# Kernel tuning notes

Hardware: AMD Instinct MI355X
Metric: run time of the kernel (lower is better)

The kernel has to match this reference:

```python
import jax, jax.numpy as jnp
import numpy as np
from jax import lax

PAD = 1  # 3x3 conv, stride 1, padding 1


def conv2d(x, w, b=None):
    # x: [B,C,H,W], w: [O,I,3,3]
    y = lax.conv_general_dilated(x, w, window_strides=(1, 1),
                                 padding=((PAD, PAD), (PAD, PAD)),
                                 dimension_numbers=("NCHW", "OIHW", "NCHW"))
    if b is not None:
        y = y + b[None, :, None, None]
    return y


def _bilinear(img, py, px):
    # img: [C,H,W]; py,px: [K,H,W] sampling coords (float). Zero padding outside.
    H, W = img.shape[1], img.shape[2]
    y0 = jnp.floor(py)
    x0 = jnp.floor(px)
    wy = py - y0  # [K,H,W]
    wx = px - x0
    y0i = y0.astype(jnp.int32)
    x0i = x0.astype(jnp.int32)

    def gather(yi, xi):
        valid = ((yi >= 0) & (yi < H) & (xi >= 0) & (xi < W)).astype(img.dtype)
        yc = jnp.clip(yi, 0, H - 1)
        xc = jnp.clip(xi, 0, W - 1)
        return img[:, yc, xc] * valid[None]  # [C,K,H,W]

    v00 = gather(y0i, x0i)
    v01 = gather(y0i, x0i + 1)
    v10 = gather(y0i + 1, x0i)
    v11 = gather(y0i + 1, x0i + 1)
    return (v00 * (1 - wy) * (1 - wx) + v01 * (1 - wy) * wx
            + v10 * wy * (1 - wx) + v11 * wy * wx)  # [C,K,H,W]


def reference(x, w_offset, b_offset, w_mask, b_mask, w_conv):
    B, C, H, W = x.shape
    K = 9  # 3x3 kernel taps
    offset = conv2d(x, w_offset, b_offset)              # [B,2K,H,W]
    mask = jax.nn.sigmoid(conv2d(x, w_mask, b_mask))    # [B,K,H,W]

    off = offset.reshape(B, K, 2, H, W)
    dy = off[:, :, 0]  # [B,K,H,W] (torchvision layout: y first)
    dx = off[:, :, 1]

    k = jnp.arange(K)
    ky = (k // 3).astype(x.dtype) - PAD  # tap row offset in {-1,0,1}
    kx = (k % 3).astype(x.dtype) - PAD
    ii = jnp.arange(H, dtype=x.dtype)
    jj = jnp.arange(W, dtype=x.dtype)

    py = ii[None, None, :, None] + ky[None, :, None, None] + dy  # [B,K,H,W]
    px = jj[None, None, None, :] + kx[None, :, None, None] + dx

    sampled = jax.vmap(_bilinear)(x, py, px)  # [B,C,K,H,W]
    sampled = sampled * mask[:, None]          # modulated deform-conv v2

    # weight [64,3,3,3] -> [O,C,K]; contract over C and kernel taps
    out = jnp.einsum('bckhw,ock->bohw', sampled, w_conv.reshape(w_conv.shape[0], C, K))
    return out


def setup_inputs() -> dict:
    key = jax.random.key(0)
    k = jax.random.split(key, 6)
    B, C, H, W = 16, 3, 256, 256
    return {
        'x': jax.random.normal(k[0], (B, C, H, W), jnp.float32),
        'w_offset': jax.random.normal(k[1], (18, 3, 3, 3), jnp.float32) * 0.1,
        'b_offset': jax.random.normal(k[2], (18,), jnp.float32) * 0.1,
        'w_mask': jax.random.normal(k[3], (9, 3, 3, 3), jnp.float32) * 0.1,
        'b_mask': jax.random.normal(k[4], (9,), jnp.float32) * 0.1,
        'w_conv': jax.random.normal(k[5], (64, 3, 3, 3), jnp.float32) * 0.1,
    }
```

## Files before the change

### kernel.cpp

```cpp
#include <hip/hip_runtime.h>
#include <hip/hip_bf16.h>

#define HH 256
#define WW 256
#define CC 3
#define KK 9
#define OC 64
#define KD 27
#define PSTS 40
#define WRB 5120
#define XST (4 * WRB)
#define XSLOT 1024
#define ROWS 2
#define SLOTS 8

typedef __attribute__((ext_vector_type(8))) short bf16x8;
typedef __attribute__((ext_vector_type(4))) short s16x4;
typedef __attribute__((ext_vector_type(4))) float f32x4;
typedef __attribute__((ext_vector_type(2))) float f32x2;
typedef __attribute__((ext_vector_type(2))) unsigned int u32x2;
typedef __attribute__((ext_vector_type(4))) unsigned int u32x4;

static __device__ __forceinline__ short f2bf(float f) {
    __hip_bfloat16 h = __float2bfloat16(f);
    return __builtin_bit_cast(short, h);
}
static __device__ __forceinline__ unsigned pack2(short a, short b) {
    return (unsigned)(unsigned short)a | ((unsigned)(unsigned short)b << 16);
}
static __device__ __forceinline__ float bf2f(unsigned w) {
    return __uint_as_float(w << 16);
}
static __device__ __forceinline__ float bfup(unsigned w) {
    return __uint_as_float(w & 0xffff0000u);
}
static __device__ __forceinline__ unsigned q8(float z) {
    float s = 1.0f / (1.0f + __expf(-z));
    return (unsigned)__builtin_rintf(s * 255.0f);
}

__global__ __launch_bounds__(256) void dcn_prep(
    const float* __restrict__ x,
    const float* __restrict__ w_offset, const float* __restrict__ b_offset,
    const float* __restrict__ w_mask,   const float* __restrict__ b_mask,
    const float* __restrict__ w_conv,
    short* __restrict__ xbf, short* __restrict__ wcf, char* __restrict__ wof,
    int npix)
{
    const int tid = threadIdx.x;
    if (blockIdx.x == gridDim.x - 1) {
        if (tid < 64) {
            const int fm = tid & 15, kc = tid >> 4;
#pragma unroll
            for (int t = 0; t < 4; ++t) {
                bf16x8 v;
#pragma unroll
                for (int e = 0; e < 8; ++e) {
                    int kd = kc * 8 + e;
                    v[e] = (kd < KD) ? f2bf(w_conv[(t * 16 + fm) * KD + kd]) : (short)0;
                }
                *(bf16x8*)(wcf + tid * 32 + t * 8) = v;
            }
#pragma unroll
            for (int t = 0; t < 2; ++t) {
                int ch = t * 16 + fm;
                bf16x8 vh, vl;
#pragma unroll
                for (int e = 0; e < 8; ++e) {
                    int kd = kc * 8 + e;
                    float val = 0.0f;
                    if (kd < KD) {
                        if (ch < 18) val = w_offset[ch * KD + kd];
                        else if (ch < KD) val = w_mask[(ch - 18) * KD + kd];
                    }
                    unsigned u = __float_as_uint(val);
                    vh[e] = (short)(u >> 16);
                    float d = val - __uint_as_float(u & 0xffff0000u);
                    vl[e] = (short)(__float_as_uint(d) >> 16);
                }
                *(bf16x8*)(wof + tid * 96 + t * 16) = vh;
                *(bf16x8*)(wof + tid * 96 + 32 + t * 16) = vl;
            }
#pragma unroll
            for (int t = 0; t < 2; ++t) {
                f32x4 cb;
#pragma unroll
                for (int r = 0; r < 4; ++r) {
                    int ch = t * 16 + kc * 4 + r;
                    float v = 0.0f;
                    if (ch < 18) v = b_offset[ch];
                    else if (ch < KD) v = b_mask[ch - 18];
                    cb[r] = v;
                }
                *(f32x4*)(wof + tid * 96 + 64 + t * 16) = cb;
            }
        }
        return;
    }

    const int p0 = (blockIdx.x * 256 + tid) * 4;
    if (p0 >= npix) return;
    const int bb = p0 >> 16;
    const int q  = p0 & 0xffff;
    const float* xb = x + (size_t)bb * (3 * 65536) + q;
    f32x4 r0 = *(const f32x4*)(xb);
    f32x4 r1 = *(const f32x4*)(xb + 65536);
    f32x4 r2 = *(const f32x4*)(xb + 131072);

    bf16x8 v0 = {f2bf(r0[0]), f2bf(r1[0]), f2bf(r2[0]), 0,
                 f2bf(r0[1]), f2bf(r1[1]), f2bf(r2[1]), 0};
    bf16x8 v1 = {f2bf(r0[2]), f2bf(r1[2]), f2bf(r2[2]), 0,
                 f2bf(r0[3]), f2bf(r1[3]), f2bf(r2[3]), 0};
    short* A = xbf + (size_t)p0 * 4;
    *(bf16x8*)A       = v0;
    *(bf16x8*)(A + 8) = v1;
}

__global__ __launch_bounds__(256, 4) void dcn_main(
    const float* __restrict__ x,
    const short* __restrict__ xbf,
    const short* __restrict__ wcf,
    const char*  __restrict__ wof,
    float* __restrict__ out)
{
    __shared__ __align__(16) char LDSBUF[XST + SLOTS * XSLOT * 2];

    const int tid = threadIdx.x;
    const int j = tid;
    const int r0 = (blockIdx.x & 127) * ROWS;
    const int b = blockIdx.x >> 7;
    const int lane = tid & 63;
    const int wv = tid >> 6;
    const int fm = lane & 15;
    const int kc = lane >> 4;

    char* wbase = LDSBUF + wv * WRB;
    short* patchS = (short*)wbase;
    short* xs = (short*)(LDSBUF + XST);

    const float* xb = x + (size_t)b * (CC * HH * WW);
    const short* xrow = xbf + (size_t)b * (HH * WW * 4);

    {
        u32x2 st[SLOTS];
#pragma unroll
        for (int s = 0; s < SLOTS; ++s) {
            int gr = min(max(r0 - 3 + s, 0), HH - 1);
            st[s] = *(const u32x2*)(xrow + ((size_t)gr * WW + tid) * 4);
        }
#pragma unroll
        for (int s = 0; s < SLOTS; ++s) {
            *(u32x2*)(xs + s * XSLOT + tid * 4) = st[s];
        }
    }
    __syncthreads();

    const char* wl = wof + lane * 96;
    bf16x8 whi0 = *(const bf16x8*)(wl);
    bf16x8 whi1 = *(const bf16x8*)(wl + 16);
    bf16x8 wlo0 = *(const bf16x8*)(wl + 32);
    bf16x8 wlo1 = *(const bf16x8*)(wl + 48);
    f32x4 cb0 = *(const f32x4*)(wl + 64);
    f32x4 cb1 = *(const f32x4*)(wl + 80);
    bf16x8 afrag[4];
#pragma unroll
    for (int t2 = 0; t2 < 4; ++t2) afrag[t2] = *(const bf16x8*)(wcf + lane * 32 + t2 * 8);

    const float* x0p = xb;
    const float* x1p = xb + (size_t)HH * WW;
    const float* x2p = xb + (size_t)2 * HH * WW;

#pragma unroll 1
    for (int d = 0; d < ROWS; ++d) {
        const int ri = r0 + d;

        const bool yok0 = (ri - 1) >= 0, yok2 = (ri + 1) < HH;
        const bool xok0 = (j - 1) >= 0, xok2 = (j + 1) < WW;
        s16x4 pr[3][3];
#pragma unroll
        for (int p = 0; p < 3; ++p) {
#pragma unroll
            for (int q = 0; q < 3; ++q) {
                int xx = min(max(j + q - 1, 0), WW - 1);
                pr[p][q] = *(const s16x4*)(xs + (d + p + 2) * XSLOT + xx * 4);
            }
        }
        {
            short* rp = patchS + lane * PSTS;
#pragma unroll
            for (int o = 0; o < 4; ++o) {
                bf16x8 vh;
#pragma unroll
                for (int e = 0; e < 8; ++e) {
                    int kd = o * 8 + e;
                    if (kd < KD) {
                        int c = kd / 9, rem = kd - c * 9, p = rem / 3, q = rem - p * 3;
                        bool ok = (p == 0 ? yok0 : (p == 2 ? yok2 : true)) &&
                                  (q == 0 ? xok0 : (q == 2 ? xok2 : true));
                        vh[e] = ok ? pr[p][q][c] : (short)0;
                    } else {
                        vh[e] = (short)0;
                    }
                }
                *(bf16x8*)(rp + o * 8) = vh;
            }
        }

        f32x4 dacc[4][2];
#pragma unroll
        for (int g = 0; g < 4; ++g) {
            bf16x8 phi = *(const bf16x8*)(patchS + (g * 16 + fm) * PSTS + kc * 8);
            f32x4 a0 = __builtin_amdgcn_mfma_f32_16x16x32_bf16(whi0, phi, cb0, 0, 0, 0);
            a0 = __builtin_amdgcn_mfma_f32_16x16x32_bf16(wlo0, phi, a0, 0, 0, 0);
            f32x4 a1 = __builtin_amdgcn_mfma_f32_16x16x32_bf16(whi1, phi, cb1, 0, 0, 0);
            a1 = __builtin_amdgcn_mfma_f32_16x16x32_bf16(wlo1, phi, a1, 0, 0, 0);
            dacc[g][0] = a0;
            dacc[g][1] = a1;
        }
#pragma unroll
        for (int g = 0; g < 4; ++g) {
            int r = g * 16 + fm;
            char* dr = wbase + r * 80;
            *(f32x4*)(dr + kc * 16) = dacc[g][0];
            f32x4 a1 = dacc[g][1];
            if (kc == 0) {
                *(unsigned*)(dr + 64) = pack2(f2bf(a1[0]), f2bf(a1[1]));
                *(unsigned short*)(dr + 68) = (unsigned short)(q8(a1[2]) | (q8(a1[3]) << 8));
            } else if (kc == 1) {
                *(unsigned short*)(dr + 70) = (unsigned short)(q8(a1[0]) | (q8(a1[1]) << 8));
                *(unsigned short*)(dr + 72) = (unsigned short)(q8(a1[2]) | (q8(a1[3]) << 8));
            } else if (kc == 2) {
                *(unsigned short*)(dr + 74) = (unsigned short)(q8(a1[0]) | (q8(a1[1]) << 8));
                *(unsigned short*)(dr + 76) = (unsigned short)q8(a1[2]);
            }
        }

        const char* myD = wbase + lane * 80;
        f32x4 d03 = *(const f32x4*)(myD);
        f32x4 d47 = *(const f32x4*)(myD + 16);
        f32x4 d8b = *(const f32x4*)(myD + 32);
        f32x4 dcf = *(const f32x4*)(myD + 48);
        u32x4 tail = *(const u32x4*)(myD + 64);

        const float dyv[9] = {d03[0], d03[2], d47[0], d47[2], d8b[0], d8b[2], dcf[0], dcf[2],
                              bf2f(tail.x)};
        const float dxv[9] = {d03[1], d03[3], d47[1], d47[3], d8b[1], d8b[3], dcf[1], dcf[3],
                              bfup(tail.x)};
        const unsigned mqv[9] = {tail.y & 255u, (tail.y >> 8) & 255u, (tail.y >> 16) & 255u,
                                 tail.y >> 24, tail.z & 255u, (tail.z >> 8) & 255u,
                                 (tail.z >> 16) & 255u, tail.z >> 24, tail.w & 255u};

        float s27[KD];
#pragma unroll
        for (int k = 0; k < KK; ++k) {
            float dy = dyv[k], dx = dxv[k];
            float msk = (float)mqv[k] * (1.0f / 255.0f);

            float py = (float)(ri + (k / 3) - 1) + dy;
            float px = (float)(j + (k % 3) - 1) + dx;
            float y0f = floorf(py), x0f = floorf(px);
            float wy = py - y0f, wx = px - x0f;
            int y0 = (int)y0f, x0 = (int)x0f;
            int y1 = y0 + 1, x1 = x0 + 1;

            float w00 = (1.0f - wy) * (1.0f - wx);
            float w01 = (1.0f - wy) * wx;
            float w10 = wy * (1.0f - wx);
            float w11 = wy * wx;

            bool v0y = (unsigned)y0 < HH, v1y = (unsigned)y1 < HH;
            bool v0x = (unsigned)x0 < WW, v1x = (unsigned)x1 < WW;
            float f00 = (v0y && v0x) ? w00 : 0.0f;
            float f01 = (v0y && v1x) ? w01 : 0.0f;
            float f10 = (v1y && v0x) ? w10 : 0.0f;
            float f11 = (v1y && v1x) ? w11 : 0.0f;

            int y0c = min(max(y0, 0), HH - 1), y1c = min(max(y1, 0), HH - 1);
            int s0 = y0c - r0 + 3;
            int s1 = y1c - r0 + 3;
            float r0v_, r1v_, r2v_;
            if (__builtin_expect(__any(((unsigned)s0 > (SLOTS - 1)) ||
                                       ((unsigned)s1 > (SLOTS - 1))), 0)) {
                int x0c = min(max(x0, 0), WW - 1), x1c = min(max(x1, 0), WW - 1);
                int o00 = y0c * WW + x0c, o01 = y0c * WW + x1c;
                int o10 = y1c * WW + x0c, o11 = y1c * WW + x1c;
                r0v_ = x0p[o00] * f00 + x0p[o01] * f01 + x0p[o10] * f10 + x0p[o11] * f11;
                r1v_ = x1p[o00] * f00 + x1p[o01] * f01 + x1p[o10] * f10 + x1p[o11] * f11;
                r2v_ = x2p[o00] * f00 + x2p[o01] * f01 + x2p[o10] * f10 + x2p[o11] * f11;
            } else {
                int xl = min(max(x0, 0), WW - 2);
                bool sw = (x0 != xl);
                const short* p0 = xs + s0 * XSLOT + xl * 4;
                const short* p1 = xs + s1 * XSLOT + xl * 4;
                u32x2 lo0 = *(const u32x2*)p0;
                u32x2 hi0 = *(const u32x2*)(p0 + 4);
                u32x2 lo1 = *(const u32x2*)p1;
                u32x2 hi1 = *(const u32x2*)(p1 + 4);

                float a0 = sw ? f01 : f00, b0 = sw ? f00 : f01;
                float a1w = sw ? f11 : f10, b1w = sw ? f10 : f11;

                r0v_ = fmaf(bf2f(lo0.x), a0, fmaf(bf2f(hi0.x), b0,
                       fmaf(bf2f(lo1.x), a1w, bf2f(hi1.x) * b1w)));
                r1v_ = fmaf(bfup(lo0.x), a0, fmaf(bfup(hi0.x), b0,
                       fmaf(bfup(lo1.x), a1w, bfup(hi1.x) * b1w)));
                r2v_ = fmaf(bf2f(lo0.y), a0, fmaf(bf2f(hi0.y), b0,
                       fmaf(bf2f(lo1.y), a1w, bf2f(hi1.y) * b1w)));
            }
            s27[k]      = r0v_ * msk;
            s27[9 + k]  = r1v_ * msk;
            s27[18 + k] = r2v_ * msk;
        }

        {
            short* srow = patchS + lane * PSTS;
#pragma unroll
            for (int o = 0; o < 4; ++o) {
                bf16x8 v;
#pragma unroll
                for (int e = 0; e < 8; ++e) {
                    int kd = o * 8 + e;
                    v[e] = (kd < KD) ? f2bf(s27[kd]) : (short)0;
                }
                *(bf16x8*)(srow + o * 8) = v;
            }
        }

        float* obase = out + ((size_t)b * OC * HH + ri) * WW;
#pragma unroll
        for (int g = 0; g < 4; ++g) {
            bf16x8 sfrag = *(const bf16x8*)(patchS + (g * 16 + fm) * PSTS + kc * 8);
#pragma unroll
            for (int t2 = 0; t2 < 4; ++t2) {
                f32x4 acc = (f32x4){0.f, 0.f, 0.f, 0.f};
                acc = __builtin_amdgcn_mfma_f32_16x16x32_bf16(sfrag, afrag[t2], acc, 0, 0, 0);
                float* op = obase + (size_t)(t2 * 16 + fm) * (HH * WW) + (wv * 64 + g * 16 + kc * 4);
                *(f32x4*)op = acc;
            }
        }
    }
}

extern "C" void kernel_launch(void* const* d_in, const int* in_sizes, int n_in,
                              void* d_out, int out_size, void* d_ws, size_t ws_size,
                              hipStream_t stream) {
    const float* x        = (const float*)d_in[0];
    const float* w_offset = (const float*)d_in[1];
    const float* b_offset = (const float*)d_in[2];
    const float* w_mask   = (const float*)d_in[3];
    const float* b_mask   = (const float*)d_in[4];
    const float* w_conv   = (const float*)d_in[5];
    float* out = (float*)d_out;

    int B = in_sizes[0] / (CC * HH * WW);
    int npix = B * HH * WW;

    short* xbf = (short*)d_ws;
    short* wcf = (short*)((char*)d_ws + (size_t)npix * 8);
    char*  wof = (char*)d_ws + (size_t)npix * 8 + 4096;

    int nb = (npix + 1023) / 1024;
    hipLaunchKernelGGL(dcn_prep, dim3(nb + 1), dim3(256), 0, stream,
                       x, w_offset, b_offset, w_mask, b_mask, w_conv,
                       xbf, wcf, wof, npix);
    hipLaunchKernelGGL(dcn_main, dim3(B * (HH / ROWS)), dim3(256), 0, stream,
                       x, xbf, wcf, wof, out);
}
```

Before: 72.37 us.

## Process both rows concurrently with 512-thread blocks instead of a serial row loop

Before, each 256-thread block handled two output rows in a serial loop. Now blocks have 512 threads and each half of the block handles one row, so the row loop is gone. The halo load is split so each half stages four of the eight LDS slots. Per-wave scratch in LDS doubles to cover eight waves, which raises shared memory per block. Larger blocks with more LDS may reduce how many blocks fit on a CU, trading serial latency inside a block for more parallelism within it.

```diff
diff --git a/kernel.cpp b/kernel.cpp
--- a/kernel.cpp
+++ b/kernel.cpp
@@ -9,9 +9,9 @@
 #define KD 27
 #define PSTS 40
 #define WRB 5120
-#define XST (4 * WRB)
+#define NWAVES 8
+#define XST (NWAVES * WRB)
 #define XSLOT 1024
-#define ROWS 2
 #define SLOTS 8
 
 typedef __attribute__((ext_vector_type(8))) short bf16x8;
@@ -75,8 +75,8 @@
                     }
                     unsigned u = __float_as_uint(val);
                     vh[e] = (short)(u >> 16);
-                    float d = val - __uint_as_float(u & 0xffff0000u);
-                    vl[e] = (short)(__float_as_uint(d) >> 16);
+                    float dd = val - __uint_as_float(u & 0xffff0000u);
+                    vl[e] = (short)(__float_as_uint(dd) >> 16);
                 }
                 *(bf16x8*)(wof + tid * 96 + t * 16) = vh;
                 *(bf16x8*)(wof + tid * 96 + 32 + t * 16) = vl;
@@ -116,7 +116,7 @@
     *(bf16x8*)(A + 8) = v1;
 }
 
-__global__ __launch_bounds__(256, 4) void dcn_main(
+__global__ __launch_bounds__(512, 4) void dcn_main(
     const float* __restrict__ x,
     const short* __restrict__ xbf,
     const short* __restrict__ wcf,
@@ -126,9 +126,11 @@
     __shared__ __align__(16) char LDSBUF[XST + SLOTS * XSLOT * 2];
 
     const int tid = threadIdx.x;
-    const int j = tid;
-    const int r0 = (blockIdx.x & 127) * ROWS;
+    const int d = tid >> 8;
+    const int j = tid & 255;
+    const int r0 = (blockIdx.x & 127) * 2;
     const int b = blockIdx.x >> 7;
+    const int ri = r0 + d;
     const int lane = tid & 63;
     const int wv = tid >> 6;
     const int fm = lane & 15;
@@ -142,15 +144,16 @@
     const short* xrow = xbf + (size_t)b * (HH * WW * 4);
 
     {
-        u32x2 st[SLOTS];
-#pragma unroll
-        for (int s = 0; s < SLOTS; ++s) {
-            int gr = min(max(r0 - 3 + s, 0), HH - 1);
-            st[s] = *(const u32x2*)(xrow + ((size_t)gr * WW + tid) * 4);
-        }
-#pragma unroll
-        for (int s = 0; s < SLOTS; ++s) {
-            *(u32x2*)(xs + s * XSLOT + tid * 4) = st[s];
+        u32x2 st[4];
+#pragma unroll
+        for (int s = 0; s < 4; ++s) {
+            int slot = d * 4 + s;
+            int gr = min(max(r0 - 3 + slot, 0), HH - 1);
+            st[s] = *(const u32x2*)(xrow + ((size_t)gr * WW + j) * 4);
+        }
+#pragma unroll
+        for (int s = 0; s < 4; ++s) {
+            *(u32x2*)(xs + (d * 4 + s) * XSLOT + j * 4) = st[s];
         }
     }
     __syncthreads();
@@ -170,10 +173,7 @@
     const float* x1p = xb + (size_t)HH * WW;
     const float* x2p = xb + (size_t)2 * HH * WW;
 
-#pragma unroll 1
-    for (int d = 0; d < ROWS; ++d) {
-        const int ri = r0 + d;
-
+    {
         const bool yok0 = (ri - 1) >= 0, yok2 = (ri + 1) < HH;
         const bool xok0 = (j - 1) >= 0, xok2 = (j + 1) < WW;
         s16x4 pr[3][3];
@@ -185,158 +185,156 @@
                 pr[p][q] = *(const s16x4*)(xs + (d + p + 2) * XSLOT + xx * 4);
             }
         }
-        {
-            short* rp = patchS + lane * PSTS;
-#pragma unroll
-            for (int o = 0; o < 4; ++o) {
-                bf16x8 vh;
-#pragma unroll
-                for (int e = 0; e < 8; ++e) {
-                    int kd = o * 8 + e;
-                    if (kd < KD) {
-                        int c = kd / 9, rem = kd - c * 9, p = rem / 3, q = rem - p * 3;
-                        bool ok = (p == 0 ? yok0 : (p == 2 ? yok2 : true)) &&
-                                  (q == 0 ? xok0 : (q == 2 ? xok2 : true));
-                        vh[e] = ok ? pr[p][q][c] : (short)0;
-                    } else {
-                        vh[e] = (short)0;
-                    }
+        short* rp = patchS + lane * PSTS;
+#pragma unroll
+        for (int o = 0; o < 4; ++o) {
+            bf16x8 vh;
+#pragma unroll
+            for (int e = 0; e < 8; ++e) {
+                int kd = o * 8 + e;
+                if (kd < KD) {
+                    int c = kd / 9, rem = kd - c * 9, p = rem / 3, q = rem - p * 3;
+                    bool ok = (p == 0 ? yok0 : (p == 2 ? yok2 : true)) &&
+                              (q == 0 ? xok0 : (q == 2 ? xok2 : true));
+                    vh[e] = ok ? pr[p][q][c] : (short)0;
+                } else {
+                    vh[e] = (short)0;
                 }
-                *(bf16x8*)(rp + o * 8) = vh;
-            }
-        }
-
-        f32x4 dacc[4][2];
-#pragma unroll
-        for (int g = 0; g < 4; ++g) {
-            bf16x8 phi = *(const bf16x8*)(patchS + (g * 16 + fm) * PSTS + kc * 8);
-            f32x4 a0 = __builtin_amdgcn_mfma_f32_16x16x32_bf16(whi0, phi, cb0, 0, 0, 0);
-            a0 = __builtin_amdgcn_mfma_f32_16x16x32_bf16(wlo0, phi, a0, 0, 0, 0);
-            f32x4 a1 = __builtin_amdgcn_mfma_f32_16x16x32_bf16(whi1, phi, cb1, 0, 0, 0);
-            a1 = __builtin_amdgcn_mfma_f32_16x16x32_bf16(wlo1, phi, a1, 0, 0, 0);
-            dacc[g][0] = a0;
-            dacc[g][1] = a1;
-        }
-#pragma unroll
-        for (int g = 0; g < 4; ++g) {
-            int r = g * 16 + fm;
-            char* dr = wbase + r * 80;
-            *(f32x4*)(dr + kc * 16) = dacc[g][0];
-            f32x4 a1 = dacc[g][1];
-            if (kc == 0) {
-                *(unsigned*)(dr + 64) = pack2(f2bf(a1[0]), f2bf(a1[1]));
-                *(unsigned short*)(dr + 68) = (unsigned short)(q8(a1[2]) | (q8(a1[3]) << 8));
-            } else if (kc == 1) {
-                *(unsigned short*)(dr + 70) = (unsigned short)(q8(a1[0]) | (q8(a1[1]) << 8));
-                *(unsigned short*)(dr + 72) = (unsigned short)(q8(a1[2]) | (q8(a1[3]) << 8));
-            } else if (kc == 2) {
-                *(unsigned short*)(dr + 74) = (unsigned short)(q8(a1[0]) | (q8(a1[1]) << 8));
-                *(unsigned short*)(dr + 76) = (unsigned short)q8(a1[2]);
-            }
-        }
-
-        const char* myD = wbase + lane * 80;
-        f32x4 d03 = *(const f32x4*)(myD);
-        f32x4 d47 = *(const f32x4*)(myD + 16);
-        f32x4 d8b = *(const f32x4*)(myD + 32);
-        f32x4 dcf = *(const f32x4*)(myD + 48);
-        u32x4 tail = *(const u32x4*)(myD + 64);
-
-        const float dyv[9] = {d03[0], d03[2], d47[0], d47[2], d8b[0], d8b[2], dcf[0], dcf[2],
-                              bf2f(tail.x)};
-        const float dxv[9] = {d03[1], d03[3], d47[1], d47[3], d8b[1], d8b[3], dcf[1], dcf[3],
-                              bfup(tail.x)};
-        const unsigned mqv[9] = {tail.y & 255u, (tail.y >> 8) & 255u, (tail.y >> 16) & 255u,
-                                 tail.y >> 24, tail.z & 255u, (tail.z >> 8) & 255u,
-                                 (tail.z >> 16) & 255u, tail.z >> 24, tail.w & 255u};
-
-        float s27[KD];
-#pragma unroll
-        for (int k = 0; k < KK; ++k) {
-            float dy = dyv[k], dx = dxv[k];
-            float msk = (float)mqv[k] * (1.0f / 255.0f);
-
-            float py = (float)(ri + (k / 3) - 1) + dy;
-            float px = (float)(j + (k % 3) - 1) + dx;
-            float y0f = floorf(py), x0f = floorf(px);
-            float wy = py - y0f, wx = px - x0f;
-            int y0 = (int)y0f, x0 = (int)x0f;
-            int y1 = y0 + 1, x1 = x0 + 1;
-
-            float w00 = (1.0f - wy) * (1.0f - wx);
-            float w01 = (1.0f - wy) * wx;
-            float w10 = wy * (1.0f - wx);
-            float w11 = wy * wx;
-
-            bool v0y = (unsigned)y0 < HH, v1y = (unsigned)y1 < HH;
-            bool v0x = (unsigned)x0 < WW, v1x = (unsigned)x1 < WW;
-            float f00 = (v0y && v0x) ? w00 : 0.0f;
-            float f01 = (v0y && v1x) ? w01 : 0.0f;
-            float f10 = (v1y && v0x) ? w10 : 0.0f;
-            float f11 = (v1y && v1x) ? w11 : 0.0f;
-
-            int y0c = min(max(y0, 0), HH - 1), y1c = min(max(y1, 0), HH - 1);
-            int s0 = y0c - r0 + 3;
-            int s1 = y1c - r0 + 3;
-            float r0v_, r1v_, r2v_;
-            if (__builtin_expect(__any(((unsigned)s0 > (SLOTS - 1)) ||
-                                       ((unsigned)s1 > (SLOTS - 1))), 0)) {
-                int x0c = min(max(x0, 0), WW - 1), x1c = min(max(x1, 0), WW - 1);
-                int o00 = y0c * WW + x0c, o01 = y0c * WW + x1c;
-                int o10 = y1c * WW + x0c, o11 = y1c * WW + x1c;
-                r0v_ = x0p[o00] * f00 + x0p[o01] * f01 + x0p[o10] * f10 + x0p[o11] * f11;
-                r1v_ = x1p[o00] * f00 + x1p[o01] * f01 + x1p[o10] * f10 + x1p[o11] * f11;
-                r2v_ = x2p[o00] * f00 + x2p[o01] * f01 + x2p[o10] * f10 + x2p[o11] * f11;
-            } else {
-                int xl = min(max(x0, 0), WW - 2);
-                bool sw = (x0 != xl);
-                const short* p0 = xs + s0 * XSLOT + xl * 4;
-                const short* p1 = xs + s1 * XSLOT + xl * 4;
-                u32x2 lo0 = *(const u32x2*)p0;
-                u32x2 hi0 = *(const u32x2*)(p0 + 4);
-                u32x2 lo1 = *(const u32x2*)p1;
-                u32x2 hi1 = *(const u32x2*)(p1 + 4);
-
-                float a0 = sw ? f01 : f00, b0 = sw ? f00 : f01;
-                float a1w = sw ? f11 : f10, b1w = sw ? f10 : f11;
-
-                r0v_ = fmaf(bf2f(lo0.x), a0, fmaf(bf2f(hi0.x), b0,
-                       fmaf(bf2f(lo1.x), a1w, bf2f(hi1.x) * b1w)));
-                r1v_ = fmaf(bfup(lo0.x), a0, fmaf(bfup(hi0.x), b0,
-                       fmaf(bfup(lo1.x), a1w, bfup(hi1.x) * b1w)));
-                r2v_ = fmaf(bf2f(lo0.y), a0, fmaf(bf2f(hi0.y), b0,
-                       fmaf(bf2f(lo1.y), a1w, bf2f(hi1.y) * b1w)));
-            }
-            s27[k]      = r0v_ * msk;
-            s27[9 + k]  = r1v_ * msk;
-            s27[18 + k] = r2v_ * msk;
-        }
-
-        {
-            short* srow = patchS + lane * PSTS;
-#pragma unroll
-            for (int o = 0; o < 4; ++o) {
-                bf16x8 v;
-#pragma unroll
-                for (int e = 0; e < 8; ++e) {
-                    int kd = o * 8 + e;
-                    v[e] = (kd < KD) ? f2bf(s27[kd]) : (short)0;
-                }
-                *(bf16x8*)(srow + o * 8) = v;
-            }
-        }
-
-        float* obase = out + ((size_t)b * OC * HH + ri) * WW;
-#pragma unroll
-        for (int g = 0; g < 4; ++g) {
-            bf16x8 sfrag = *(const bf16x8*)(patchS + (g * 16 + fm) * PSTS + kc * 8);
-#pragma unroll
-            for (int t2 = 0; t2 < 4; ++t2) {
-                f32x4 acc = (f32x4){0.f, 0.f, 0.f, 0.f};
-                acc = __builtin_amdgcn_mfma_f32_16x16x32_bf16(sfrag, afrag[t2], acc, 0, 0, 0);
-                float* op = obase + (size_t)(t2 * 16 + fm) * (HH * WW) + (wv * 64 + g * 16 + kc * 4);
-                *(f32x4*)op = acc;
-            }
+            }
+            *(bf16x8*)(rp + o * 8) = vh;
+        }
+    }
+
+    f32x4 dacc[4][2];
+#pragma unroll
+    for (int g = 0; g < 4; ++g) {
+        bf16x8 phi = *(const bf16x8*)(patchS + (g * 16 + fm) * PSTS + kc * 8);
+        f32x4 a0 = __builtin_amdgcn_mfma_f32_16x16x32_bf16(whi0, phi, cb0, 0, 0, 0);
+        a0 = __builtin_amdgcn_mfma_f32_16x16x32_bf16(wlo0, phi, a0, 0, 0, 0);
+        f32x4 a1 = __builtin_amdgcn_mfma_f32_16x16x32_bf16(whi1, phi, cb1, 0, 0, 0);
+        a1 = __builtin_amdgcn_mfma_f32_16x16x32_bf16(wlo1, phi, a1, 0, 0, 0);
+        dacc[g][0] = a0;
+        dacc[g][1] = a1;
+    }
+#pragma unroll
+    for (int g = 0; g < 4; ++g) {
+        int r = g * 16 + fm;
+        char* dr = wbase + r * 80;
+        *(f32x4*)(dr + kc * 16) = dacc[g][0];
+        f32x4 a1 = dacc[g][1];
+        if (kc == 0) {
+            *(unsigned*)(dr + 64) = pack2(f2bf(a1[0]), f2bf(a1[1]));
+            *(unsigned short*)(dr + 68) = (unsigned short)(q8(a1[2]) | (q8(a1[3]) << 8));
+        } else if (kc == 1) {
+            *(unsigned short*)(dr + 70) = (unsigned short)(q8(a1[0]) | (q8(a1[1]) << 8));
+            *(unsigned short*)(dr + 72) = (unsigned short)(q8(a1[2]) | (q8(a1[3]) << 8));
+        } else if (kc == 2) {
+            *(unsigned short*)(dr + 74) = (unsigned short)(q8(a1[0]) | (q8(a1[1]) << 8));
+            *(unsigned short*)(dr + 76) = (unsigned short)q8(a1[2]);
+        }
+    }
+
+    const char* myD = wbase + lane * 80;
+    f32x4 d03 = *(const f32x4*)(myD);
+    f32x4 d47 = *(const f32x4*)(myD + 16);
+    f32x4 d8b = *(const f32x4*)(myD + 32);
+    f32x4 dcf = *(const f32x4*)(myD + 48);
+    u32x4 tail = *(const u32x4*)(myD + 64);
+
+    const float dyv[9] = {d03[0], d03[2], d47[0], d47[2], d8b[0], d8b[2], dcf[0], dcf[2],
+                          bf2f(tail.x)};
+    const float dxv[9] = {d03[1], d03[3], d47[1], d47[3], d8b[1], d8b[3], dcf[1], dcf[3],
+                          bfup(tail.x)};
+    const unsigned mqv[9] = {tail.y & 255u, (tail.y >> 8) & 255u, (tail.y >> 16) & 255u,
+                             tail.y >> 24, tail.z & 255u, (tail.z >> 8) & 255u,
+                             (tail.z >> 16) & 255u, tail.z >> 24, tail.w & 255u};
+
+    float s27[KD];
+#pragma unroll
+    for (int k = 0; k < KK; ++k) {
+        float dy = dyv[k], dx = dxv[k];
+        float msk = (float)mqv[k] * (1.0f / 255.0f);
+
+        float py = (float)(ri + (k / 3) - 1) + dy;
+        float px = (float)(j + (k % 3) - 1) + dx;
+        float y0f = floorf(py), x0f = floorf(px);
+        float wy = py - y0f, wx = px - x0f;
+        int y0 = (int)y0f, x0 = (int)x0f;
+        int y1 = y0 + 1, x1 = x0 + 1;
+
+        float w00 = (1.0f - wy) * (1.0f - wx);
+        float w01 = (1.0f - wy) * wx;
+        float w10 = wy * (1.0f - wx);
+        float w11 = wy * wx;
+
+        bool v0y = (unsigned)y0 < HH, v1y = (unsigned)y1 < HH;
+        bool v0x = (unsigned)x0 < WW, v1x = (unsigned)x1 < WW;
+        float f00 = (v0y && v0x) ? w00 : 0.0f;
+        float f01 = (v0y && v1x) ? w01 : 0.0f;
+        float f10 = (v1y && v0x) ? w10 : 0.0f;
+        float f11 = (v1y && v1x) ? w11 : 0.0f;
+
+        int y0c = min(max(y0, 0), HH - 1), y1c = min(max(y1, 0), HH - 1);
+        int s0 = y0c - r0 + 3;
+        int s1 = y1c - r0 + 3;
+        float r0v_, r1v_, r2v_;
+        if (__builtin_expect(__any(((unsigned)s0 > (SLOTS - 1)) ||
+                                   ((unsigned)s1 > (SLOTS - 1))), 0)) {
+            int x0c = min(max(x0, 0), WW - 1), x1c = min(max(x1, 0), WW - 1);
+            int o00 = y0c * WW + x0c, o01 = y0c * WW + x1c;
+            int o10 = y1c * WW + x0c, o11 = y1c * WW + x1c;
+            r0v_ = x0p[o00] * f00 + x0p[o01] * f01 + x0p[o10] * f10 + x0p[o11] * f11;
+            r1v_ = x1p[o00] * f00 + x1p[o01] * f01 + x1p[o10] * f10 + x1p[o11] * f11;
+            r2v_ = x2p[o00] * f00 + x2p[o01] * f01 + x2p[o10] * f10 + x2p[o11] * f11;
+        } else {
+            int xl = min(max(x0, 0), WW - 2);
+            bool sw = (x0 != xl);
+            const short* p0 = xs + s0 * XSLOT + xl * 4;
+            const short* p1 = xs + s1 * XSLOT + xl * 4;
+            u32x2 lo0 = *(const u32x2*)p0;
+            u32x2 hi0 = *(const u32x2*)(p0 + 4);
+            u32x2 lo1 = *(const u32x2*)p1;
+            u32x2 hi1 = *(const u32x2*)(p1 + 4);
+
+            float a0 = sw ? f01 : f00, b0 = sw ? f00 : f01;
+            float a1w = sw ? f11 : f10, b1w = sw ? f10 : f11;
+
+            r0v_ = fmaf(bf2f(lo0.x), a0, fmaf(bf2f(hi0.x), b0,
+                   fmaf(bf2f(lo1.x), a1w, bf2f(hi1.x) * b1w)));
+            r1v_ = fmaf(bfup(lo0.x), a0, fmaf(bfup(hi0.x), b0,
+                   fmaf(bfup(lo1.x), a1w, bfup(hi1.x) * b1w)));
+            r2v_ = fmaf(bf2f(lo0.y), a0, fmaf(bf2f(hi0.y), b0,
+                   fmaf(bf2f(lo1.y), a1w, bf2f(hi1.y) * b1w)));
+        }
+        s27[k]      = r0v_ * msk;
+        s27[9 + k]  = r1v_ * msk;
+        s27[18 + k] = r2v_ * msk;
+    }
+
+    {
+        short* srow = patchS + lane * PSTS;
+#pragma unroll
+        for (int o = 0; o < 4; ++o) {
+            bf16x8 v;
+#pragma unroll
+            for (int e = 0; e < 8; ++e) {
+                int kd = o * 8 + e;
+                v[e] = (kd < KD) ? f2bf(s27[kd]) : (short)0;
+            }
+            *(bf16x8*)(srow + o * 8) = v;
+        }
+    }
+
+    float* obase = out + ((size_t)b * OC * HH + ri) * WW;
+#pragma unroll
+    for (int g = 0; g < 4; ++g) {
+        bf16x8 sfrag = *(const bf16x8*)(patchS + (g * 16 + fm) * PSTS + kc * 8);
+#pragma unroll
+        for (int t2 = 0; t2 < 4; ++t2) {
+            f32x4 acc = (f32x4){0.f, 0.f, 0.f, 0.f};
+            acc = __builtin_amdgcn_mfma_f32_16x16x32_bf16(sfrag, afrag[t2], acc, 0, 0, 0);
+            float* op = obase + (size_t)(t2 * 16 + fm) * (HH * WW) + ((wv & 3) * 64 + g * 16 + kc * 4);
+            *(f32x4*)op = acc;
         }
     }
 }
@@ -363,6 +361,6 @@
     hipLaunchKernelGGL(dcn_prep, dim3(nb + 1), dim3(256), 0, stream,
                        x, w_offset, b_offset, w_mask, b_mask, w_conv,
                        xbf, wcf, wof, npix);
-    hipLaunchKernelGGL(dcn_main, dim3(B * (HH / ROWS)), dim3(256), 0, stream,
+    hipLaunchKernelGGL(dcn_main, dim3(B * (HH / 2)), dim3(512), 0, stream,
                        x, xbf, wcf, wof, out);
 }
```

New measurement: 78.85 us. 9.0% more time.
